# Performance work log

Hardware: AMD Instinct MI355X
Metric: run time of the kernel (lower is better)

Reference implementation:

```python
import jax, jax.numpy as jnp
import numpy as np

N = 100_000      # nodes
E = 1_600_000    # edges
D = 128          # dim_in == dim_h
L = 3            # num_layers
G = 512          # num graphs in batch
EPS = 1e-5       # BatchNorm1d eps


def setup_inputs() -> dict:
    key = jax.random.key(0)
    k1, k2, k3, k4 = jax.random.split(key, 4)
    x = jax.random.normal(k1, (N, D), dtype=jnp.float32)
    edge_index = jax.random.randint(k2, (2, E), 0, N, dtype=jnp.int64)
    batch = jnp.sort(jax.random.randint(k3, (N,), 0, G, dtype=jnp.int64))
    Ws = jax.random.normal(k4, (L, D, D), dtype=jnp.float32) * 0.05
    bs = jnp.zeros((L, D), dtype=jnp.float32)
    gammas = jnp.ones((L, D), dtype=jnp.float32)
    betas = jnp.zeros((L, D), dtype=jnp.float32)
    return {"x": x, "edge_index": edge_index, "batch": batch,
            "Ws": Ws, "bs": bs, "gammas": gammas, "betas": betas}


def reference(x, edge_index, batch, Ws, bs, gammas, betas):
    src, dst = edge_index[0], edge_index[1]
    # GCN symmetric normalization with self-loops (PyG GCNConv default):
    # deg counts incoming edges at dst, +1 for the self-loop.
    deg = jnp.zeros((N,), dtype=x.dtype).at[dst].add(1.0) + 1.0
    inv_sqrt = jax.lax.rsqrt(deg)
    edge_coeff = inv_sqrt[src] * inv_sqrt[dst]   # [E]
    self_coeff = inv_sqrt * inv_sqrt             # [N] self-loop weight deg^-1

    h = x
    for i in range(L):
        hw = h @ Ws[i]                                           # [N, D]
        agg = (jnp.zeros_like(hw).at[dst].add(hw[src] * edge_coeff[:, None])
               + hw * self_coeff[:, None] + bs[i])               # [N, D]
        # BatchNorm1d (training-mode batch statistics, biased variance)
        mean = agg.mean(axis=0)
        var = agg.var(axis=0)
        hn = (agg - mean) * jax.lax.rsqrt(var + EPS) * gammas[i] + betas[i]
        h = jax.nn.relu(hn)

    # global_add_pool: scatter-add node features by graph id
    return jax.ops.segment_sum(h, batch, num_segments=G)        # [G, D]
```

## Files before the change

### kernel.cpp

```cpp
#include <hip/hip_runtime.h>

#define D 128
#define CHUNK 512
#define NSLICE 8
#define SLW 16

using short8 = __attribute__((ext_vector_type(8))) short;
using f32x4  = __attribute__((ext_vector_type(4))) float;
using f32x2  = __attribute__((ext_vector_type(2))) float;
using u32x2  = __attribute__((ext_vector_type(2))) unsigned;

__device__ __forceinline__ unsigned short f2bf(float f){
  unsigned u = __builtin_bit_cast(unsigned, f);
  u += 0x7fffu + ((u >> 16) & 1u);
  return (unsigned short)(u >> 16);
}
__device__ __forceinline__ float bflo2f(unsigned v){
  return __builtin_bit_cast(float, v << 16);
}
__device__ __forceinline__ float bfhi2f(unsigned v){
  return __builtin_bit_cast(float, v & 0xffff0000u);
}
__device__ __forceinline__ float bfs2f(unsigned short v){
  return __builtin_bit_cast(float, ((unsigned)v) << 16);
}
__device__ __forceinline__ unsigned cvtpk(float lo, float hi){
  unsigned r;
  asm("v_cvt_pk_bf16_f32 %0, %1, %2" : "=v"(r) : "v"(lo), "v"(hi));
  return r;
}

__global__ void k_deg(const int* __restrict__ dst, int* __restrict__ deg,
                      int* __restrict__ rank, int E){
  int e = blockIdx.x * 256 + threadIdx.x;
  if (e < E) rank[e] = atomicAdd(&deg[dst[e]], 1);
}

__global__ void k_chunksum(const int* __restrict__ deg, int* __restrict__ csum, int n){
  __shared__ int s[256];
  int tid = threadIdx.x;
  int n0 = blockIdx.x * CHUNK + tid * 2;
  int v = 0;
  if (n0     < n) v += deg[n0];
  if (n0 + 1 < n) v += deg[n0 + 1];
  s[tid] = v; __syncthreads();
  for (int off = 128; off > 0; off >>= 1){
    if (tid < off) s[tid] += s[tid + off];
    __syncthreads();
  }
  if (tid == 0) csum[blockIdx.x] = s[0];
}

__global__ void k_scanchunks(int* __restrict__ csum, int nchunks){
  __shared__ int s[256];
  int tid = threadIdx.x;
  int v = (tid < nchunks) ? csum[tid] : 0;
  s[tid] = v; __syncthreads();
  for (int off = 1; off < 256; off <<= 1){
    int t = (tid >= off) ? s[tid - off] : 0;
    __syncthreads();
    s[tid] += t;
    __syncthreads();
  }
  if (tid < nchunks) csum[tid] = s[tid] - v;
}

__global__ void k_offsets(const int* __restrict__ deg, const int* __restrict__ csum,
                          int* __restrict__ offs, float* __restrict__ inv, int n){
  __shared__ int s[256];
  int tid = threadIdx.x;
  int n0 = blockIdx.x * CHUNK + tid * 2;
  int d0 = (n0     < n) ? deg[n0]     : 0;
  int d1 = (n0 + 1 < n) ? deg[n0 + 1] : 0;
  int pair = d0 + d1;
  s[tid] = pair; __syncthreads();
  for (int off = 1; off < 256; off <<= 1){
    int t = (tid >= off) ? s[tid - off] : 0;
    __syncthreads();
    s[tid] += t;
    __syncthreads();
  }
  int excl = s[tid] - pair + csum[blockIdx.x];
  if (n0     <= n) offs[n0]     = excl;
  if (n0 + 1 <= n) offs[n0 + 1] = excl + d0;
  if (n0     < n) inv[n0]     = rsqrtf((float)(d0 + 1));
  if (n0 + 1 < n) inv[n0 + 1] = rsqrtf((float)(d1 + 1));
}

__global__ __launch_bounds__(256)
void k_csrfill(const int* __restrict__ src, const int* __restrict__ dst,
               const int* __restrict__ offs, const int* __restrict__ rank,
               int* __restrict__ csrc, int E, int n){
  int part = blockIdx.x & 7;
  int blk  = blockIdx.x >> 3;
  int nblk = gridDim.x >> 3;
  int per = (n + 7) / 8;
  int d0 = part * per, d1 = min(d0 + per, n);
  int stride = nblk * 256;
  for (int e = blk * 256 + threadIdx.x; e < E; e += stride){
    int d = dst[e];
    if (d >= d0 && d < d1){
      csrc[offs[d] + rank[e]] = src[e];
    }
  }
}

#define WSTRIDE 136
__global__ __launch_bounds__(512)
void k_gemm(const float* __restrict__ hf, const unsigned short* __restrict__ hb,
            const float* __restrict__ W, const float* __restrict__ inv,
            const float* __restrict__ stats, const float* __restrict__ gamma,
            const float* __restrict__ beta, float invn,
            int do_norm, unsigned short* __restrict__ hwS, int nrows){
  __shared__ unsigned short Wt[128 * WSTRIDE];
  __shared__ float s_sc[128], s_sh[128];
  int tid = threadIdx.x;
  if (do_norm && tid < 128){
    float mean = stats[tid] * invn;
    float var = stats[128 + tid] * invn - mean * mean;
    float isd = rsqrtf(var + 1e-5f);
    float sc = gamma[tid] * isd;
    s_sc[tid] = sc;
    s_sh[tid] = beta[tid] - mean * sc;
  }
  for (int i = tid; i < 128 * 128; i += 512){
    int k = i >> 7, c = i & 127;
    Wt[c * WSTRIDE + k] = f2bf(W[i]);
  }
  __syncthreads();

  int wave = tid >> 6, lane = tid & 63;
  int r0 = blockIdx.x * 128 + wave * 16;
  int row = r0 + (lane & 15);
  int kg = lane >> 4;
  int rowc = row < nrows ? row : nrows - 1;

  short8 a[4];
  if (do_norm){
#pragma unroll
    for (int kt = 0; kt < 4; ++kt){
      int k0 = kt * 32 + kg * 8;
      int sl = k0 >> 4, o = k0 & 15;
      short8 raw = *(const short8*)(hb + ((long)sl * nrows + rowc) * SLW + o);
      unsigned u[4];
#pragma unroll
      for (int j = 0; j < 4; ++j){
        float lo = bfs2f((unsigned short)raw[2*j]);
        float hi = bfs2f((unsigned short)raw[2*j+1]);
        lo = fmaxf(0.f, lo * s_sc[k0+2*j]   + s_sh[k0+2*j]);
        hi = fmaxf(0.f, hi * s_sc[k0+2*j+1] + s_sh[k0+2*j+1]);
        u[j] = cvtpk(lo, hi);
      }
      a[kt] = *(short8*)u;
    }
  } else {
    const float* hrow = hf + (long)rowc * D;
#pragma unroll
    for (int kt = 0; kt < 4; ++kt){
      int k0 = kt * 32 + kg * 8;
      f32x4 v0 = *(const f32x4*)(hrow + k0);
      f32x4 v1 = *(const f32x4*)(hrow + k0 + 4);
      unsigned u[4];
      u[0] = cvtpk(v0[0], v0[1]);
      u[1] = cvtpk(v0[2], v0[3]);
      u[2] = cvtpk(v1[0], v1[1]);
      u[3] = cvtpk(v1[2], v1[3]);
      a[kt] = *(short8*)u;
    }
  }

  f32x4 acc[8] = {};
#pragma unroll
  for (int ct = 0; ct < 8; ++ct){
    int col = ct * 16 + (lane & 15);
    const unsigned short* bp = &Wt[col * WSTRIDE + kg * 8];
#pragma unroll
    for (int kt = 0; kt < 4; ++kt){
      short8 b = *(const short8*)(bp + kt * 32);
      acc[ct] = __builtin_amdgcn_mfma_f32_16x16x32_bf16(a[kt], b, acc[ct], 0, 0, 0);
    }
  }

  int colbase = lane & 15;
  int rowo = r0 + kg * 4;
  float ivr[4];
#pragma unroll
  for (int r = 0; r < 4; ++r) ivr[r] = inv[min(rowo + r, nrows - 1)];
#pragma unroll
  for (int ct = 0; ct < 8; ++ct){
#pragma unroll
    for (int r = 0; r < 4; ++r){
      int rr = rowo + r;
      if (rr < nrows)
        hwS[((long)ct * nrows + rr) * SLW + colbase] = f2bf(acc[ct][r] * ivr[r]);
    }
  }
}

__global__ __launch_bounds__(256)
void k_agg(const unsigned short* __restrict__ hwS, const float* __restrict__ inv,
           const int* __restrict__ offs, const int* __restrict__ csrc,
           const float* __restrict__ bias,
           unsigned* __restrict__ aggS, float* __restrict__ stats, int n,
           int ngroups){
  int g   = blockIdx.x & 7;
  int grp = blockIdx.x >> 3;
  int tid = threadIdx.x, lane = tid & 63, wv = tid >> 6;
  int ns = lane >> 2;
  int cp = lane & 3;
  int nwaves = ngroups * 4;
  int gw = grp * 4 + wv;
  int per = (n + nwaves - 1) / nwaves;
  per = (per + 15) & ~15;
  int n0 = min(gw * per, n), n1 = min(n0 + per, n);

  const u32x2* slice2 = (const u32x2*)((const unsigned*)hwS + (long)g * n * 8);
  u32x2* oslice2 = (u32x2*)(aggS + (long)g * n * 8);

  int cb = g * 16 + cp * 4;
  float b0 = bias[cb], b1 = bias[cb + 1], b2 = bias[cb + 2], b3 = bias[cb + 3];
  float s0 = 0, s1 = 0, s2 = 0, s3 = 0;
  float q0 = 0, q1 = 0, q2 = 0, q3 = 0;

  for (int base = n0; base < n1; base += 16){
    int node = base + ns;
    bool act = node < n1;
    int ndc = act ? node : n1 - 1;
    int e  = offs[ndc];
    int ee = offs[ndc + 1];
    float a0 = 0, a1 = 0, a2 = 0, a3 = 0;

    int i0 = csrc[(e     < ee) ? e     : 0];
    int i1 = csrc[(e + 1 < ee) ? e + 1 : 0];
    int i2 = csrc[(e + 2 < ee) ? e + 2 : 0];
    int i3 = csrc[(e + 3 < ee) ? e + 3 : 0];
    while (__any(e < ee)){
      int j0 = csrc[(e + 4 < ee) ? e + 4 : 0];
      int j1 = csrc[(e + 5 < ee) ? e + 5 : 0];
      int j2 = csrc[(e + 6 < ee) ? e + 6 : 0];
      int j3 = csrc[(e + 7 < ee) ? e + 7 : 0];
      u32x2 v0 = slice2[(long)i0 * 4 + cp];
      u32x2 v1 = slice2[(long)i1 * 4 + cp];
      u32x2 v2 = slice2[(long)i2 * 4 + cp];
      u32x2 v3 = slice2[(long)i3 * 4 + cp];
      bool k0 = e < ee, k1 = e + 1 < ee, k2 = e + 2 < ee, k3 = e + 3 < ee;
      v0[0] = k0 ? v0[0] : 0u; v0[1] = k0 ? v0[1] : 0u;
      v1[0] = k1 ? v1[0] : 0u; v1[1] = k1 ? v1[1] : 0u;
      v2[0] = k2 ? v2[0] : 0u; v2[1] = k2 ? v2[1] : 0u;
      v3[0] = k3 ? v3[0] : 0u; v3[1] = k3 ? v3[1] : 0u;
      a0 += (bflo2f(v0[0]) + bflo2f(v1[0])) + (bflo2f(v2[0]) + bflo2f(v3[0]));
      a1 += (bfhi2f(v0[0]) + bfhi2f(v1[0])) + (bfhi2f(v2[0]) + bfhi2f(v3[0]));
      a2 += (bflo2f(v0[1]) + bflo2f(v1[1])) + (bflo2f(v2[1]) + bflo2f(v3[1]));
      a3 += (bfhi2f(v0[1]) + bfhi2f(v1[1])) + (bfhi2f(v2[1]) + bfhi2f(v3[1]));
      i0 = j0; i1 = j1; i2 = j2; i3 = j3;
      e += 4;
    }

    if (act){
      u32x2 sv = slice2[(long)node * 4 + cp];
      float ivd = inv[node];
      a0 = (a0 + bflo2f(sv[0])) * ivd + b0;
      a1 = (a1 + bfhi2f(sv[0])) * ivd + b1;
      a2 = (a2 + bflo2f(sv[1])) * ivd + b2;
      a3 = (a3 + bfhi2f(sv[1])) * ivd + b3;
      u32x2 pk;
      pk[0] = ((unsigned)f2bf(a1) << 16) | (unsigned)f2bf(a0);
      pk[1] = ((unsigned)f2bf(a3) << 16) | (unsigned)f2bf(a2);
      __builtin_nontemporal_store(pk, oslice2 + (long)node * 4 + cp);
      s0 += a0; s1 += a1; s2 += a2; s3 += a3;
      q0 += a0 * a0; q1 += a1 * a1; q2 += a2 * a2; q3 += a3 * a3;
    }
  }

#pragma unroll
  for (int off = 4; off <= 32; off <<= 1){
    s0 += __shfl_xor(s0, off, 64); s1 += __shfl_xor(s1, off, 64);
    s2 += __shfl_xor(s2, off, 64); s3 += __shfl_xor(s3, off, 64);
    q0 += __shfl_xor(q0, off, 64); q1 += __shfl_xor(q1, off, 64);
    q2 += __shfl_xor(q2, off, 64); q3 += __shfl_xor(q3, off, 64);
  }

  __shared__ float red[4][4][8];
  if (ns == 0){
    red[wv][cp][0] = s0; red[wv][cp][1] = s1;
    red[wv][cp][2] = s2; red[wv][cp][3] = s3;
    red[wv][cp][4] = q0; red[wv][cp][5] = q1;
    red[wv][cp][6] = q2; red[wv][cp][7] = q3;
  }
  __syncthreads();
  if (tid < 4){
    float t[8] = {0,0,0,0,0,0,0,0};
#pragma unroll
    for (int w = 0; w < 4; ++w)
#pragma unroll
      for (int j = 0; j < 8; ++j) t[j] += red[w][tid][j];
    int c = g * 16 + tid * 4;
#pragma unroll
    for (int j = 0; j < 4; ++j){
      atomicAdd(&stats[c + j],       t[j]);
      atomicAdd(&stats[128 + c + j], t[4 + j]);
    }
  }
}

__global__ __launch_bounds__(256)
void k_pool(const unsigned* __restrict__ aggS, const float* __restrict__ stats,
            const float* __restrict__ gamma, const float* __restrict__ beta,
            float invn, const int* __restrict__ batch,
            float* __restrict__ out, int n){
  __shared__ float psc[128], psh[128];
  int tid = threadIdx.x, lane = tid & 63, wv = tid >> 6;
  if (tid < 128){
    float mean = stats[tid] * invn;
    float var = stats[128 + tid] * invn - mean * mean;
    float isd = rsqrtf(var + 1e-5f);
    float sc = gamma[tid] * isd;
    psc[tid] = sc;
    psh[tid] = beta[tid] - mean * sc;
  }
  __syncthreads();
  int gw = blockIdx.x * 4 + wv;
  int n0 = gw * 64;
  if (n0 >= n) return;
  int n1 = min(n0 + 64, n);
  int c0 = lane * 2;
  int sl = lane >> 3, cp = lane & 7;
  long sbase = (long)sl * n * 8;
  float sc0 = psc[c0], sc1 = psc[c0 + 1];
  float sh0 = psh[c0], sh1 = psh[c0 + 1];
  int g = batch[n0];
  float a0 = 0, a1 = 0;
  for (int nd = n0; nd < n1; ++nd){
    int gn = batch[nd];
    if (gn != g){
      atomicAdd(&out[(long)g * D + c0],     a0);
      atomicAdd(&out[(long)g * D + c0 + 1], a1);
      a0 = 0; a1 = 0; g = gn;
    }
    unsigned v = aggS[sbase + (long)nd * 8 + cp];
    a0 += fmaxf(0.f, bflo2f(v) * sc0 + sh0);
    a1 += fmaxf(0.f, bfhi2f(v) * sc1 + sh1);
  }
  atomicAdd(&out[(long)g * D + c0],     a0);
  atomicAdd(&out[(long)g * D + c0 + 1], a1);
}

extern "C" void kernel_launch(void* const* d_in, const int* in_sizes, int n_in,
                              void* d_out, int out_size, void* d_ws, size_t ws_size,
                              hipStream_t stream){
  const float* x      = (const float*)d_in[0];
  const int*   ei     = (const int*)d_in[1];
  const int*   batch  = (const int*)d_in[2];
  const float* Ws     = (const float*)d_in[3];
  const float* bs     = (const float*)d_in[4];
  const float* gammas = (const float*)d_in[5];
  const float* betas  = (const float*)d_in[6];

  const int E_ = in_sizes[1] / 2;
  const int N_ = in_sizes[2];
  const int* src = ei;
  const int* dst = ei + E_;

  char* p = (char*)d_ws;
  auto alloc = [&](size_t bytes) -> void* {
    void* r = (void*)p;
    p += (bytes + 255) & ~(size_t)255;
    return r;
  };
  unsigned*       bufA   = (unsigned*)      alloc((size_t)N_ * D * 2);
  unsigned short* hwS    = (unsigned short*)alloc((size_t)N_ * D * 2);
  int*            deg    = (int*)           alloc((size_t)N_ * 4);
  float*          inv    = (float*)         alloc((size_t)N_ * 4);
  int*            offs   = (int*)           alloc((size_t)(N_ + 1) * 4);
  int*            rank   = (int*)           alloc((size_t)E_ * 4);
  int*            csrc   = (int*)           alloc((size_t)E_ * 4);
  float*          stats  = (float*)         alloc(3 * 256 * 4);
  int*            csum   = (int*)           alloc(256 * 4);

  hipMemsetAsync(deg,    0, (size_t)N_ * 4, stream);
  hipMemsetAsync(stats,  0, 3 * 256 * 4, stream);
  hipMemsetAsync(d_out,  0, (size_t)out_size * 4, stream);

  float invn = 1.0f / (float)N_;
  int nchunks = (N_ + CHUNK - 1) / CHUNK;
  k_deg       <<<(E_ + 255) / 256, 256, 0, stream>>>(dst, deg, rank, E_);
  k_chunksum  <<<nchunks, 256, 0, stream>>>(deg, csum, N_);
  k_scanchunks<<<1, 256, 0, stream>>>(csum, nchunks);
  k_offsets   <<<nchunks, 256, 0, stream>>>(deg, csum, offs, inv, N_);
  k_csrfill   <<<2048, 256, 0, stream>>>(src, dst, offs, rank, csrc, E_, N_);

  int gemm_blocks = (N_ + 127) / 128;
  int ngroups = 256;
  for (int l = 0; l < 3; ++l){
    const float* st = (l == 0) ? stats : stats + (size_t)(l - 1) * 256;
    const float* gm = (l == 0) ? gammas : gammas + (size_t)(l - 1) * D;
    const float* bt = (l == 0) ? betas : betas + (size_t)(l - 1) * D;
    k_gemm<<<gemm_blocks, 512, 0, stream>>>(x, (const unsigned short*)bufA,
                                            Ws + (size_t)l * D * D, inv,
                                            st, gm, bt, invn,
                                            (l == 0) ? 0 : 1, hwS, N_);
    k_agg<<<ngroups * 8, 256, 0, stream>>>(hwS, inv, offs, csrc, bs + (size_t)l * D,
                                           bufA, stats + (size_t)l * 256, N_, ngroups);
  }
  k_pool<<<(N_ + 255) / 256, 256, 0, stream>>>(bufA, stats + 2 * 256,
                                               gammas + 2 * D, betas + 2 * D, invn,
                                               batch, (float*)d_out, N_);
}
```

Before: 489.5 us.

## Pad CSR rows to multiples of four with a zero sentinel node

Each node's CSR row is padded to a multiple of four entries (always at least one pad). The pad entries point to an extra zero row appended to every hw slice, so the aggregation loop no longer needs per-edge bounds selects or masking of gathered values. The cost is about 4N more index entries to store, two small extra kernels (pad fill and zero row), and redundant gathers of the sentinel row.

```diff
diff --git a/kernel.cpp b/kernel.cpp
--- a/kernel.cpp
+++ b/kernel.cpp
@@ -29,6 +29,8 @@
   asm("v_cvt_pk_bf16_f32 %0, %1, %2" : "=v"(r) : "v"(lo), "v"(hi));
   return r;
 }
+
+__device__ __forceinline__ int plen4(int d){ return (d + 4) & ~3; }
 
 __global__ void k_deg(const int* __restrict__ dst, int* __restrict__ deg,
                       int* __restrict__ rank, int E){
@@ -41,8 +43,8 @@
   int tid = threadIdx.x;
   int n0 = blockIdx.x * CHUNK + tid * 2;
   int v = 0;
-  if (n0     < n) v += deg[n0];
-  if (n0 + 1 < n) v += deg[n0 + 1];
+  if (n0     < n) v += plen4(deg[n0]);
+  if (n0 + 1 < n) v += plen4(deg[n0 + 1]);
   s[tid] = v; __syncthreads();
   for (int off = 128; off > 0; off >>= 1){
     if (tid < off) s[tid] += s[tid + off];
@@ -72,7 +74,9 @@
   int n0 = blockIdx.x * CHUNK + tid * 2;
   int d0 = (n0     < n) ? deg[n0]     : 0;
   int d1 = (n0 + 1 < n) ? deg[n0 + 1] : 0;
-  int pair = d0 + d1;
+  int p0 = (n0     < n) ? plen4(d0) : 0;
+  int p1 = (n0 + 1 < n) ? plen4(d1) : 0;
+  int pair = p0 + p1;
   s[tid] = pair; __syncthreads();
   for (int off = 1; off < 256; off <<= 1){
     int t = (tid >= off) ? s[tid - off] : 0;
@@ -82,9 +86,24 @@
   }
   int excl = s[tid] - pair + csum[blockIdx.x];
   if (n0     <= n) offs[n0]     = excl;
-  if (n0 + 1 <= n) offs[n0 + 1] = excl + d0;
+  if (n0 + 1 <= n) offs[n0 + 1] = excl + p0;
   if (n0     < n) inv[n0]     = rsqrtf((float)(d0 + 1));
   if (n0 + 1 < n) inv[n0 + 1] = rsqrtf((float)(d1 + 1));
+}
+
+__global__ void k_fillpad(const int* __restrict__ deg, const int* __restrict__ offs,
+                          int* __restrict__ csrc, int n){
+  int i = blockIdx.x * 256 + threadIdx.x;
+  if (i >= n) return;
+  int s = offs[i] + deg[i];
+  int e = offs[i + 1];
+  for (int j = s; j < e; ++j) csrc[j] = n;
+}
+
+__global__ void k_zrow(unsigned short* __restrict__ hwS, int n){
+  int tid = threadIdx.x;
+  int sl = tid >> 4, c = tid & 15;
+  hwS[((long)sl * (n + 1) + n) * 16 + c] = 0;
 }
 
 __global__ __launch_bounds__(256)
@@ -192,7 +211,7 @@
     for (int r = 0; r < 4; ++r){
       int rr = rowo + r;
       if (rr < nrows)
-        hwS[((long)ct * nrows + rr) * SLW + colbase] = f2bf(acc[ct][r] * ivr[r]);
+        hwS[((long)ct * (nrows + 1) + rr) * SLW + colbase] = f2bf(acc[ct][r] * ivr[r]);
     }
   }
 }
@@ -214,7 +233,7 @@
   per = (per + 15) & ~15;
   int n0 = min(gw * per, n), n1 = min(n0 + per, n);
 
-  const u32x2* slice2 = (const u32x2*)((const unsigned*)hwS + (long)g * n * 8);
+  const u32x2* slice2 = (const u32x2*)((const unsigned*)hwS + (long)g * (n + 1) * 8);
   u32x2* oslice2 = (u32x2*)(aggS + (long)g * n * 8);
 
   int cb = g * 16 + cp * 4;
@@ -228,26 +247,22 @@
     int ndc = act ? node : n1 - 1;
     int e  = offs[ndc];
     int ee = offs[ndc + 1];
+    int em = ee - 1;
     float a0 = 0, a1 = 0, a2 = 0, a3 = 0;
 
-    int i0 = csrc[(e     < ee) ? e     : 0];
-    int i1 = csrc[(e + 1 < ee) ? e + 1 : 0];
-    int i2 = csrc[(e + 2 < ee) ? e + 2 : 0];
-    int i3 = csrc[(e + 3 < ee) ? e + 3 : 0];
+    int i0 = csrc[e];
+    int i1 = csrc[e + 1];
+    int i2 = csrc[e + 2];
+    int i3 = csrc[e + 3];
     while (__any(e < ee)){
-      int j0 = csrc[(e + 4 < ee) ? e + 4 : 0];
-      int j1 = csrc[(e + 5 < ee) ? e + 5 : 0];
-      int j2 = csrc[(e + 6 < ee) ? e + 6 : 0];
-      int j3 = csrc[(e + 7 < ee) ? e + 7 : 0];
+      int j0 = csrc[min(e + 4, em)];
+      int j1 = csrc[min(e + 5, em)];
+      int j2 = csrc[min(e + 6, em)];
+      int j3 = csrc[min(e + 7, em)];
       u32x2 v0 = slice2[(long)i0 * 4 + cp];
       u32x2 v1 = slice2[(long)i1 * 4 + cp];
       u32x2 v2 = slice2[(long)i2 * 4 + cp];
       u32x2 v3 = slice2[(long)i3 * 4 + cp];
-      bool k0 = e < ee, k1 = e + 1 < ee, k2 = e + 2 < ee, k3 = e + 3 < ee;
-      v0[0] = k0 ? v0[0] : 0u; v0[1] = k0 ? v0[1] : 0u;
-      v1[0] = k1 ? v1[0] : 0u; v1[1] = k1 ? v1[1] : 0u;
-      v2[0] = k2 ? v2[0] : 0u; v2[1] = k2 ? v2[1] : 0u;
-      v3[0] = k3 ? v3[0] : 0u; v3[1] = k3 ? v3[1] : 0u;
       a0 += (bflo2f(v0[0]) + bflo2f(v1[0])) + (bflo2f(v2[0]) + bflo2f(v3[0]));
       a1 += (bfhi2f(v0[0]) + bfhi2f(v1[0])) + (bfhi2f(v2[0]) + bfhi2f(v3[0]));
       a2 += (bflo2f(v0[1]) + bflo2f(v1[1])) + (bflo2f(v2[1]) + bflo2f(v3[1]));
@@ -368,12 +383,12 @@
     return r;
   };
   unsigned*       bufA   = (unsigned*)      alloc((size_t)N_ * D * 2);
-  unsigned short* hwS    = (unsigned short*)alloc((size_t)N_ * D * 2);
+  unsigned short* hwS    = (unsigned short*)alloc((size_t)(N_ + 1) * D * 2);
   int*            deg    = (int*)           alloc((size_t)N_ * 4);
   float*          inv    = (float*)         alloc((size_t)N_ * 4);
   int*            offs   = (int*)           alloc((size_t)(N_ + 1) * 4);
   int*            rank   = (int*)           alloc((size_t)E_ * 4);
-  int*            csrc   = (int*)           alloc((size_t)E_ * 4);
+  int*            csrc   = (int*)           alloc(((size_t)E_ + 4 * N_ + 64) * 4);
   float*          stats  = (float*)         alloc(3 * 256 * 4);
   int*            csum   = (int*)           alloc(256 * 4);
 
@@ -387,7 +402,9 @@
   k_chunksum  <<<nchunks, 256, 0, stream>>>(deg, csum, N_);
   k_scanchunks<<<1, 256, 0, stream>>>(csum, nchunks);
   k_offsets   <<<nchunks, 256, 0, stream>>>(deg, csum, offs, inv, N_);
+  k_fillpad   <<<(N_ + 255) / 256, 256, 0, stream>>>(deg, offs, csrc, N_);
   k_csrfill   <<<2048, 256, 0, stream>>>(src, dst, offs, rank, csrc, E_, N_);
+  k_zrow      <<<1, 128, 0, stream>>>(hwS, N_);
 
   int gemm_blocks = (N_ + 127) / 128;
   int ngroups = 256;
```

New measurement: 520.0 us. 6.2% more time.
